# Optimization experiments

Hardware: AMD Instinct MI355X
Metric: run time of the kernel (lower is better)

Reference implementation:

```python
import jax, jax.numpy as jnp
import numpy as np
import math

NUM_HEADS = 16

def _skew(QEr):
    # QEr: [B, H, S, S] -> pad 1 on left of last dim, reshape, drop first row
    B, H, S, _ = QEr.shape
    padded = jnp.pad(QEr, ((0, 0), (0, 0), (0, 0), (1, 0)))  # [B,H,S,S+1]
    reshaped = padded.reshape(B, H, S + 1, S)
    return reshaped[:, :, 1:, :]  # [B,H,S,S]

def setup_inputs() -> dict:
    key = jax.random.key(0)
    ks = jax.random.split(key, 8)
    B, S, D, dh = 4, 1024, 1024, 64
    x = jax.random.normal(ks[0], (B, S, D), dtype=jnp.float32)
    scale = 1.0 / math.sqrt(D)
    Wq = jax.random.normal(ks[1], (D, D), dtype=jnp.float32) * scale
    Wk = jax.random.normal(ks[2], (D, D), dtype=jnp.float32) * scale
    Wv = jax.random.normal(ks[3], (D, D), dtype=jnp.float32) * scale
    bq = jnp.zeros((D,), dtype=jnp.float32)
    bk = jnp.zeros((D,), dtype=jnp.float32)
    bv = jnp.zeros((D,), dtype=jnp.float32)
    Er = jax.random.normal(ks[4], (S, dh), dtype=jnp.float32)
    return {"x": x, "Wq": Wq, "bq": bq, "Wk": Wk, "bk": bk, "Wv": Wv, "bv": bv, "Er": Er}

def reference(x, Wq, bq, Wk, bk, Wv, bv, Er):
    B, S, D = x.shape
    H = NUM_HEADS
    dh = D // H
    # Linear projections (torch Linear: x @ W.T + b)
    q = (x @ Wq.T + bq).reshape(B, S, H, dh).transpose(0, 2, 1, 3)  # [B,H,S,dh]
    k = (x @ Wk.T + bk).reshape(B, S, H, dh).transpose(0, 2, 1, 3)
    v = (x @ Wv.T + bv).reshape(B, S, H, dh).transpose(0, 2, 1, 3)
    # Relative position term: q @ Er^T then skew (start = max_len - S = 0)
    QEr = jnp.einsum('bhsd,td->bhst', q, Er)  # [B,H,S,S]
    Srel = _skew(QEr)
    QKt = jnp.einsum('bhsd,bhtd->bhst', q, k)  # [B,H,S,S]
    attn = (QKt + Srel) / math.sqrt(dh)
    causal = jnp.tril(jnp.ones((S, S), dtype=bool))
    attn = jnp.where(causal[None, None], attn, jnp.float32(-1e6))
    attn = jax.nn.softmax(attn, axis=-1)
    out = jnp.einsum('bhst,bhtd->bhsd', attn, v)  # [B,H,S,dh]
    out = out.transpose(0, 2, 1, 3).reshape(B, S, D)
    return out  # dropout is identity in eval / p=0
```

## Files before the change

kernel.cpp:

```cpp
#include <hip/hip_runtime.h>
#include <stdint.h>

#define S_LEN 1024
#define DM 1024
#define NH 16
#define DH 64
#define NB 4

typedef unsigned short u16;
typedef __attribute__((ext_vector_type(8))) short short8;
typedef __attribute__((ext_vector_type(4))) float f32x4;
typedef __attribute__((ext_vector_type(4))) unsigned int u32x4;
typedef __attribute__((ext_vector_type(4))) unsigned short u16x4;

__device__ __forceinline__ u16 f2bf(float f) {
  union { float f; unsigned int u; } c;
  c.f = f;
  unsigned int u = c.u;
  return (u16)((u + 0x7fffu + ((u >> 16) & 1u)) >> 16);
}

__device__ __forceinline__ void g2l16(const void* g, void* l) {
  __builtin_amdgcn_global_load_lds(
      (const __attribute__((address_space(1))) unsigned int*)(uintptr_t)g,
      (__attribute__((address_space(3))) unsigned int*)(uint32_t)(uintptr_t)l,
      16, 0, 0);
}

__device__ __forceinline__ float grp16_max(float v) {
  union { float f; int i; } c, o;
  c.f = v; o.i = __builtin_amdgcn_update_dpp(c.i, c.i, 0xB1, 0xF, 0xF, false);
  v = fmaxf(v, o.f);
  c.f = v; o.i = __builtin_amdgcn_update_dpp(c.i, c.i, 0x4E, 0xF, 0xF, false);
  v = fmaxf(v, o.f);
  c.f = v; o.i = __builtin_amdgcn_update_dpp(c.i, c.i, 0x124, 0xF, 0xF, false);
  v = fmaxf(v, o.f);
  c.f = v; o.i = __builtin_amdgcn_update_dpp(c.i, c.i, 0x128, 0xF, 0xF, false);
  v = fmaxf(v, o.f);
  return v;
}
__device__ __forceinline__ float grp16_sum(float v) {
  union { float f; int i; } c, o;
  c.f = v; o.i = __builtin_amdgcn_update_dpp(c.i, c.i, 0xB1, 0xF, 0xF, false);
  v += o.f;
  c.f = v; o.i = __builtin_amdgcn_update_dpp(c.i, c.i, 0x4E, 0xF, 0xF, false);
  v += o.f;
  c.f = v; o.i = __builtin_amdgcn_update_dpp(c.i, c.i, 0x124, 0xF, 0xF, false);
  v += o.f;
  c.f = v; o.i = __builtin_amdgcn_update_dpp(c.i, c.i, 0x128, 0xF, 0xF, false);
  v += o.f;
  return v;
}

__global__ __launch_bounds__(256) void cvt_f32_bf16(
    const float* __restrict__ x, const float* __restrict__ Wq,
    const float* __restrict__ Wk, const float* __restrict__ Wv,
    const float* __restrict__ Er, u16* __restrict__ xb,
    u16* __restrict__ Wqb, u16* __restrict__ Wkb, u16* __restrict__ Wvb,
    u16* __restrict__ Erb) {
  const size_t f = ((size_t)blockIdx.x * 256 + threadIdx.x) * 8;
  const float* src;
  u16* dst;
  size_t off;
  if (f < 4194304) { src = x; dst = xb; off = f; }
  else if (f < 5242880) { src = Wq; dst = Wqb; off = f - 4194304; }
  else if (f < 6291456) { src = Wk; dst = Wkb; off = f - 5242880; }
  else if (f < 7340032) { src = Wv; dst = Wvb; off = f - 6291456; }
  else { src = Er; dst = Erb; off = f - 7340032; }
  const float4 a = *(const float4*)(src + off);
  const float4 b = *(const float4*)(src + off + 4);
  u16 o[8] = {f2bf(a.x), f2bf(a.y), f2bf(a.z), f2bf(a.w),
              f2bf(b.x), f2bf(b.y), f2bf(b.z), f2bf(b.w)};
  *(u32x4*)(dst + off) = *(const u32x4*)o;
}

__global__ __launch_bounds__(256) void qkv_gemm(
    const u16* __restrict__ x,
    const u16* __restrict__ Wq, const float* __restrict__ bq,
    const u16* __restrict__ Wk, const float* __restrict__ bk,
    const u16* __restrict__ Wv, const float* __restrict__ bv,
    u16* __restrict__ Qo, u16* __restrict__ Ko, u16* __restrict__ Vo) {
  __shared__ __attribute__((aligned(16))) u16 Al[2][128 * 32];
  __shared__ __attribute__((aligned(16))) u16 Bl[2][128 * 32];

  const int tid = threadIdx.x;
  const int lane = tid & 63;
  const int wave = tid >> 6;

  const int o =
      ((int)blockIdx.z * gridDim.y + blockIdx.y) * gridDim.x + blockIdx.x;
  const int swz = (o & 7) * 96 + (o >> 3);
  const int z = swz >> 8;
  const int rem = swz & 255;
  const int m0 = (rem >> 3) * 128;
  const int n0 = (rem & 7) * 128;

  const u16* W = (z == 0) ? Wq : (z == 1) ? Wk : Wv;
  const float* bias = (z == 0) ? bq : (z == 1) ? bk : bv;

  f32x4 acc[4][4];
  const f32x4 fzero = {0.f, 0.f, 0.f, 0.f};
#pragma unroll
  for (int i = 0; i < 4; i++)
#pragma unroll
    for (int j = 0; j < 4; j++) acc[i][j] = fzero;

  const int srow = tid >> 2;
  const int schunk = tid & 3;
  const u16* gA = x + (size_t)(m0 + srow) * DM + schunk * 8;
  const u16* gB = W + (size_t)(n0 + srow) * DM + schunk * 8;

  const int fr = lane & 15;
  const int fq = lane >> 4;
  const int wr = (wave >> 1) * 64;
  const int wc = (wave & 1) * 64;

  auto stageAB = [&](int k, int bf) {
    g2l16(gA + k, &Al[bf][tid * 8]);
    g2l16(gA + (size_t)64 * DM + k, &Al[bf][2048 + tid * 8]);
    g2l16(gB + k, &Bl[bf][tid * 8]);
    g2l16(gB + (size_t)64 * DM + k, &Bl[bf][2048 + tid * 8]);
  };

  stageAB(0, 0);
  __syncthreads();
  int bf = 0;

  for (int k = 0; k < DM; k += 32) {
    if (k + 32 < DM) stageAB(k + 32, bf ^ 1);
    short8 a[4], b[4];
#pragma unroll
    for (int i = 0; i < 4; i++)
      a[i] = *(const short8*)&Al[bf][(wr + i * 16 + fr) * 32 + fq * 8];
#pragma unroll
    for (int j = 0; j < 4; j++)
      b[j] = *(const short8*)&Bl[bf][(wc + j * 16 + fr) * 32 + fq * 8];
    __builtin_amdgcn_s_setprio(1);
#pragma unroll
    for (int i = 0; i < 4; i++)
#pragma unroll
      for (int j = 0; j < 4; j++)
        acc[i][j] =
            __builtin_amdgcn_mfma_f32_16x16x32_bf16(a[i], b[j], acc[i][j], 0, 0, 0);
    __builtin_amdgcn_s_setprio(0);
    __syncthreads();
    bf ^= 1;
  }

#pragma unroll
  for (int j = 0; j < 4; j++) {
    const int n = n0 + wc + j * 16 + fr;
    const float bsv = bias[n];
    const int h = n >> 6, d = n & (DH - 1);
#pragma unroll
    for (int i = 0; i < 4; i++) {
      const int mb = m0 + wr + i * 16 + fq * 4;
      const int bb = mb >> 10, s = mb & (S_LEN - 1);
      if (z == 2) {
        u16x4 ov;
#pragma unroll
        for (int r = 0; r < 4; r++) ov[r] = f2bf(acc[i][j][r] + bsv);
        *(u16x4*)&Vo[((size_t)(bb * NH + h) * DH + d) * S_LEN + s] = ov;
      } else if (z == 1) {
#pragma unroll
        for (int r = 0; r < 4; r++)
          Ko[((size_t)(bb * NH + h) * S_LEN + s + r) * DH + d] =
              f2bf(acc[i][j][r] + bsv);
      } else {
#pragma unroll
        for (int r = 0; r < 4; r++)
          Qo[((size_t)(bb * NH + h) * S_LEN + s + r) * DH + d] =
              f2bf(acc[i][j][r] + bsv);
      }
    }
  }
}

__global__ __launch_bounds__(512, 4) void attn(
    const u16* __restrict__ Q, const u16* __restrict__ K,
    const u16* __restrict__ Vt, const u16* __restrict__ Er,
    float* __restrict__ out) {
  __shared__ __attribute__((aligned(16))) u16 Kl[2][64 * 64];
  __shared__ __attribute__((aligned(16))) u16 Vl[2][64 * 64];
  __shared__ __attribute__((aligned(16))) u16 El[256 * 64];
  __shared__ __attribute__((aligned(16))) u16 Pl[8][16 * 64];

  const int tid = threadIdx.x;
  const int lane = tid & 63;
  const int w = tid >> 6;
  const int bh = (int)blockIdx.x * 8 + ((int)blockIdx.y & 7);
  const int slot = (int)blockIdx.y >> 3;
  const int it = (slot < 4) ? slot : 11 - slot;
  const int b = bh >> 4, h = bh & (NH - 1);
  const int i0 = it * 128;
  const int jmax = i0 + 64;
  const int i0w = i0 + w * 16;
  const int E0b = S_LEN - 128 - i0;

  const u16* Qb = Q + (size_t)bh * S_LEN * DH;
  const char* Kb = (const char*)(K + (size_t)bh * S_LEN * DH);
  const char* Vb = (const char*)(Vt + (size_t)bh * DH * S_LEN);
  const char* Eb = (const char*)Er;
  u16* Pw = Pl[w];

  const int fr = lane & 15;
  const int fq = lane >> 4;
  const f32x4 fzero = {0.f, 0.f, 0.f, 0.f};

  const int r0 = tid >> 3;
  const int ch = (tid & 7) * 16;

  auto stageKV = [&](int j0, int bf) {
    const int sw = ch ^ ((r0 & 7) << 4);
    g2l16(Kb + (size_t)(j0 + r0) * 128 + sw, (char*)&Kl[bf][0] + r0 * 128 + ch);
    g2l16(Vb + (size_t)r0 * 2048 + j0 * 2 + sw,
          (char*)&Vl[bf][0] + r0 * 128 + ch);
  };
  auto stageEl = [&](int e0, int np) {
    for (int p = 0; p < np; p++) {
      const int e = e0 + p * 64 + r0;
      const int slt = e & 255;
      const int ec = (e > S_LEN - 1) ? (S_LEN - 1) : e;
      const int sw = ch ^ ((slt & 7) << 4);
      g2l16(Eb + (size_t)ec * 128 + sw, (char*)El + slt * 128 + ch);
    }
  };

  const short8 aq0 = *(const short8*)&Qb[(size_t)(i0w + fr) * DH + fq * 8];
  const short8 aq1 = *(const short8*)&Qb[(size_t)(i0w + fr) * DH + 32 + fq * 8];

  float mrow[4], lp[4];
  f32x4 accO[4];
#pragma unroll
  for (int r = 0; r < 4; r++) { mrow[r] = -3.0e38f; lp[r] = 0.f; }
#pragma unroll
  for (int t = 0; t < 4; t++) accO[t] = fzero;

  f32x4 zzc = fzero;
  const int ksw = (fr & 7) << 4;

  int buf = 0;
  stageKV(0, 0);
  stageEl(E0b, 3);
  __syncthreads();

  for (int j0 = 0; j0 <= jmax; j0 += 64) {
    if (j0 < jmax) {
      stageKV(j0 + 64, buf ^ 1);
      stageEl(E0b + j0 + 192, 1);
    }

    int tmax = (i0w + 15 - j0) >> 4;
    if (tmax > 3) tmax = 3;

    if (tmax >= 0) {
      f32x4 sfr[4];
#pragma unroll
      for (int t = 0; t < 4; t++) sfr[t] = fzero;
      __builtin_amdgcn_s_setprio(1);
#pragma unroll
      for (int t = 0; t < 4; t++)
        if (t <= tmax) {
          const char* kr = (const char*)&Kl[buf][0] + (t * 16 + fr) * 128;
          const short8 b0 = *(const short8*)(kr + ((fq * 16) ^ ksw));
          const short8 b1 = *(const short8*)(kr + ((64 + fq * 16) ^ ksw));
          f32x4 z = fzero;
          z = __builtin_amdgcn_mfma_f32_16x16x32_bf16(aq0, b0, z, 0, 0, 0);
          z = __builtin_amdgcn_mfma_f32_16x16x32_bf16(aq1, b1, z, 0, 0, 0);
          sfr[t] = z;
        }
      __builtin_amdgcn_s_setprio(0);

      const int ebs = S_LEN - 16 - i0w + j0;
      f32x4 zz[5];
#pragma unroll
      for (int f = 0; f < 5; f++) zz[f] = fzero;
      const int f0 = (j0 == 0) ? 0 : 1;
#pragma unroll
      for (int f = 0; f < 5; f++)
        if (f >= f0 && f <= tmax + 1) {
          const int slt = ((ebs + f * 16) & 255) + fr;
          const char* er = (const char*)El + slt * 128;
          const short8 b0 = *(const short8*)(er + ((fq * 16) ^ ksw));
          const short8 b1 = *(const short8*)(er + ((64 + fq * 16) ^ ksw));
          f32x4 z = fzero;
          z = __builtin_amdgcn_mfma_f32_16x16x32_bf16(aq0, b0, z, 0, 0, 0);
          z = __builtin_amdgcn_mfma_f32_16x16x32_bf16(aq1, b1, z, 0, 0, 0);
          zz[f] = z;
        }
      if (j0 > 0) zz[0] = zzc;
      zzc = zz[4];

      float p[4][4];
#pragma unroll
      for (int r = 0; r < 4; r++) {
        const int row = fq * 4 + r;
        const int c = 15 - row + fr;
        const int src = (fq << 4) | (c & 15);
        float sh[5];
#pragma unroll
        for (int f = 0; f < 5; f++) sh[f] = __shfl(zz[f][r], src);
#pragma unroll
        for (int t = 0; t < 4; t++) {
          const float rel = (c < 16) ? sh[t] : sh[t + 1];
          float sv = (sfr[t][r] + rel) * 0.125f;
          const int jj = j0 + t * 16 + fr;
          const int ii = i0w + row;
          if (jj > ii) sv = -3.0e38f;
          p[t][r] = sv;
        }
      }

#pragma unroll
      for (int r = 0; r < 4; r++) {
        float rm = fmaxf(fmaxf(p[0][r], p[1][r]), fmaxf(p[2][r], p[3][r]));
        rm = grp16_max(rm);
        const float mnew = fmaxf(mrow[r], rm);
        const float alpha = __expf(mrow[r] - mnew);
        mrow[r] = mnew;
        float rs = 0.f;
#pragma unroll
        for (int t = 0; t < 4; t++) {
          const float e = __expf(p[t][r] - mnew);
          p[t][r] = e;
          rs += e;
        }
        lp[r] = lp[r] * alpha + rs;
#pragma unroll
        for (int t = 0; t < 4; t++) accO[t][r] *= alpha;
      }

#pragma unroll
      for (int t = 0; t < 4; t++)
#pragma unroll
        for (int r = 0; r < 4; r++)
          Pw[(fq * 4 + r) * 64 + (((t ^ fq) << 4) + fr)] = f2bf(p[t][r]);
      __builtin_amdgcn_s_waitcnt(0xC07F);

      const int rsw = (fr >> 2) << 4;
      const short8 ap0 = *(const short8*)&Pw[fr * 64 + ((fq * 8) ^ rsw)];
      const short8 ap1 = *(const short8*)&Pw[fr * 64 + ((32 + fq * 8) ^ rsw)];

      __builtin_amdgcn_s_setprio(1);
#pragma unroll
      for (int t = 0; t < 4; t++) {
        const char* vr = (const char*)&Vl[buf][0] + (t * 16 + fr) * 128;
        const short8 b0 = *(const short8*)(vr + ((fq * 16) ^ ksw));
        const short8 b1 = *(const short8*)(vr + ((64 + fq * 16) ^ ksw));
        accO[t] =
            __builtin_amdgcn_mfma_f32_16x16x32_bf16(ap0, b0, accO[t], 0, 0, 0);
        accO[t] =
            __builtin_amdgcn_mfma_f32_16x16x32_bf16(ap1, b1, accO[t], 0, 0, 0);
      }
      __builtin_amdgcn_s_setprio(0);
    }

    __syncthreads();
    buf ^= 1;
  }

#pragma unroll
  for (int r = 0; r < 4; r++) {
    const float lr = grp16_sum(lp[r]);
    const float inv = 1.f / lr;
    const int s = i0w + fq * 4 + r;
#pragma unroll
    for (int t = 0; t < 4; t++) {
      const int d = t * 16 + fr;
      out[((size_t)b * S_LEN + s) * DM + h * DH + d] = accO[t][r] * inv;
    }
  }
}

extern "C" void kernel_launch(void* const* d_in, const int* in_sizes, int n_in,
                              void* d_out, int out_size, void* d_ws, size_t ws_size,
                              hipStream_t stream) {
  const float* x = (const float*)d_in[0];
  const float* Wq = (const float*)d_in[1];
  const float* bq = (const float*)d_in[2];
  const float* Wk = (const float*)d_in[3];
  const float* bk = (const float*)d_in[4];
  const float* Wv = (const float*)d_in[5];
  const float* bv = (const float*)d_in[6];
  const float* Er = (const float*)d_in[7];
  float* out = (float*)d_out;

  const size_t per = (size_t)NB * NH * S_LEN * DH;
  u16* Qw = (u16*)d_ws;
  u16* Kw = Qw + per;
  u16* Vw = Kw + per;
  u16* xb = Vw + per;
  u16* Wqb = xb + per;
  u16* Wkb = Wqb + (size_t)DM * DM;
  u16* Wvb = Wkb + (size_t)DM * DM;
  u16* Erb = Wvb + (size_t)DM * DM;

  cvt_f32_bf16<<<3616, 256, 0, stream>>>(x, Wq, Wk, Wv, Er, xb, Wqb, Wkb, Wvb,
                                         Erb);
  dim3 g1(DM / 128, (NB * S_LEN) / 128, 3);
  qkv_gemm<<<g1, dim3(256), 0, stream>>>(xb, Wqb, bq, Wkb, bk, Wvb, bv, Qw, Kw,
                                         Vw);
  dim3 g2(8, NB * NH);
  attn<<<g2, dim3(512), 0, stream>>>(Qw, Kw, Vw, Erb, out);
}
```

Measured before the change: 161.4 us.

## Triple-buffer QKV GEMM loads and use exp2 softmax with diagonal-only masking

The QKV projection GEMM goes from double to triple buffering in LDS. It prefetches two k-steps ahead and waits on vmcnt with a raw barrier instead of a full __syncthreads, so more global-load latency is hidden. In attention, the 1/8 scale is folded into a log2(e)-prescaled constant so the softmax can use the hardware exp2 directly. The causal mask is now applied only on tiles that cross the diagonal, which removes per-element compare work on interior tiles. In exchange the GEMM uses more LDS per block, and the hand-written waitcnt must correctly track the four outstanding loads per stage.

```diff
diff --git a/kernel.cpp b/kernel.cpp
--- a/kernel.cpp
+++ b/kernel.cpp
@@ -6,6 +6,8 @@
 #define NH 16
 #define DH 64
 #define NB 4
+
+#define SCL 0.18033688011112042f
 
 typedef unsigned short u16;
 typedef __attribute__((ext_vector_type(8))) short short8;
@@ -80,8 +82,8 @@
     const u16* __restrict__ Wk, const float* __restrict__ bk,
     const u16* __restrict__ Wv, const float* __restrict__ bv,
     u16* __restrict__ Qo, u16* __restrict__ Ko, u16* __restrict__ Vo) {
-  __shared__ __attribute__((aligned(16))) u16 Al[2][128 * 32];
-  __shared__ __attribute__((aligned(16))) u16 Bl[2][128 * 32];
+  __shared__ __attribute__((aligned(16))) u16 Al[3][128 * 32];
+  __shared__ __attribute__((aligned(16))) u16 Bl[3][128 * 32];
 
   const int tid = threadIdx.x;
   const int lane = tid & 63;
@@ -123,18 +125,24 @@
   };
 
   stageAB(0, 0);
-  __syncthreads();
-  int bf = 0;
-
+  stageAB(32, 1);
+  asm volatile("s_waitcnt vmcnt(4)" ::: "memory");
+  __builtin_amdgcn_s_barrier();
+
+  int cur = 0;
   for (int k = 0; k < DM; k += 32) {
-    if (k + 32 < DM) stageAB(k + 32, bf ^ 1);
+    if (k + 64 < DM) {
+      int pf = cur - 1;
+      if (pf < 0) pf += 3;
+      stageAB(k + 64, pf);
+    }
     short8 a[4], b[4];
 #pragma unroll
     for (int i = 0; i < 4; i++)
-      a[i] = *(const short8*)&Al[bf][(wr + i * 16 + fr) * 32 + fq * 8];
+      a[i] = *(const short8*)&Al[cur][(wr + i * 16 + fr) * 32 + fq * 8];
 #pragma unroll
     for (int j = 0; j < 4; j++)
-      b[j] = *(const short8*)&Bl[bf][(wc + j * 16 + fr) * 32 + fq * 8];
+      b[j] = *(const short8*)&Bl[cur][(wc + j * 16 + fr) * 32 + fq * 8];
     __builtin_amdgcn_s_setprio(1);
 #pragma unroll
     for (int i = 0; i < 4; i++)
@@ -143,8 +151,9 @@
         acc[i][j] =
             __builtin_amdgcn_mfma_f32_16x16x32_bf16(a[i], b[j], acc[i][j], 0, 0, 0);
     __builtin_amdgcn_s_setprio(0);
-    __syncthreads();
-    bf ^= 1;
+    asm volatile("s_waitcnt vmcnt(4)" ::: "memory");
+    __builtin_amdgcn_s_barrier();
+    cur = (cur == 2) ? 0 : cur + 1;
   }
 
 #pragma unroll
@@ -303,11 +312,18 @@
 #pragma unroll
         for (int t = 0; t < 4; t++) {
           const float rel = (c < 16) ? sh[t] : sh[t + 1];
-          float sv = (sfr[t][r] + rel) * 0.125f;
-          const int jj = j0 + t * 16 + fr;
-          const int ii = i0w + row;
-          if (jj > ii) sv = -3.0e38f;
-          p[t][r] = sv;
+          p[t][r] = (sfr[t][r] + rel) * SCL;
+        }
+      }
+      if (j0 + 63 > i0w) {
+#pragma unroll
+        for (int r = 0; r < 4; r++) {
+          const int ii = i0w + fq * 4 + r;
+#pragma unroll
+          for (int t = 0; t < 4; t++) {
+            const int jj = j0 + t * 16 + fr;
+            if (jj > ii) p[t][r] = -3.0e38f;
+          }
         }
       }
 
@@ -316,12 +332,12 @@
         float rm = fmaxf(fmaxf(p[0][r], p[1][r]), fmaxf(p[2][r], p[3][r]));
         rm = grp16_max(rm);
         const float mnew = fmaxf(mrow[r], rm);
-        const float alpha = __expf(mrow[r] - mnew);
+        const float alpha = __builtin_amdgcn_exp2f(mrow[r] - mnew);
         mrow[r] = mnew;
         float rs = 0.f;
 #pragma unroll
         for (int t = 0; t < 4; t++) {
-          const float e = __expf(p[t][r] - mnew);
+          const float e = __builtin_amdgcn_exp2f(p[t][r] - mnew);
           p[t][r] = e;
           rs += e;
         }
```

New measurement: 165.2 us. +2.4%, slower.
